# Performance work log

Measured on AMD Instinct MI355X. Metric: run time of the kernel, lower is better.

The kernel has to match this reference:

```python
import jax, jax.numpy as jnp
import numpy as np

X_DIM, H_DIM, Y_DIM, ROLLOUT = 256, 2048, 256, 4096


def setup_inputs() -> dict:
    key = jax.random.key(0)
    ks = jax.random.split(key, 6)
    inp = {
        "x": jax.random.normal(ks[0], (1, ROLLOUT, X_DIM), dtype=jnp.float32),
        "h": jnp.zeros((H_DIM,), dtype=jnp.float32),
        "Wc": jax.random.normal(ks[1], (X_DIM + H_DIM, H_DIM), dtype=jnp.float32) * 0.01,
        "Wu": jax.random.normal(ks[2], (X_DIM + H_DIM, H_DIM), dtype=jnp.float32) * 0.01,
        "Wr": jax.random.normal(ks[3], (X_DIM + H_DIM, H_DIM), dtype=jnp.float32) * 0.01,
        "bc": jnp.zeros((H_DIM,), dtype=jnp.float32),
        "bu": jnp.zeros((H_DIM,), dtype=jnp.float32),
        "br": jnp.zeros((H_DIM,), dtype=jnp.float32),
        "Wh_y": jax.random.normal(ks[4], (H_DIM, Y_DIM), dtype=jnp.float32) * 0.01,
        "by": jnp.zeros((Y_DIM,), dtype=jnp.float32),
    }
    return inp


def reference(x, h, Wc, Wu, Wr, bc, bu, br, Wh_y, by):
    xs = x[0]  # [T, x_dim]

    def step(hid, xt):
        xc = jnp.concatenate([xt, hid])                      # [x_dim + h_dim]
        Lu = jax.nn.sigmoid(xc @ Wu + bu)                    # update gate
        Lr = jax.nn.sigmoid(xc @ Wr + br)                    # reset gate
        xr = jnp.concatenate([xt, hid * Lr])
        c_tilda = jnp.tanh(xr @ Wc + bc)
        h_new = c_tilda * Lu + hid * (1.0 - Lu)
        y = h_new @ Wh_y + by
        return h_new, y

    h_fin, ys = jax.lax.scan(step, h, xs)  # ys: [T, y_dim]
    return ys, h_fin
```

## Files before the change

### kernel.cpp

```cpp
#include <hip/hip_runtime.h>
#include <hip/hip_bf16.h>

#define TSTEPS 4096
#define XD 256
#define HD 2048
#define YD 256
#define KD 2304
#define NWG 256
#define NT 512

#define WU_OFF 0
#define WR_OFF (8*KD*2)
#define WC_OFF (16*KD*2)
#define WY_OFF (24*KD*2)
#define V1_OFF (WY_OFF + HD*4)
#define V2_OFF (V1_OFF + KD*4)
#define RED_OFF (V2_OFF + KD*4)
#define LDS_BYTES (RED_OFF + 256)

#define HFLAGS_U32 0
#define RFLAGS_U32 8192
#define HGO_U32    16384
#define RGO_U32    16640
#define WS_ZERO_BYTES 67584
#define HB0_OFF 67584
#define HB1_OFF 75776
#define RB0_OFF 83968
#define RB1_OFF 92160

__device__ __forceinline__ float bflo(unsigned u){ return __uint_as_float(u << 16); }
__device__ __forceinline__ float bfhi(unsigned u){ return __uint_as_float(u & 0xffff0000u); }
__device__ __forceinline__ unsigned short f2bf(float f){
  unsigned b = __float_as_uint(f);
  b += 0x7fffu + ((b >> 16) & 1u);
  return (unsigned short)(b >> 16);
}
__device__ __forceinline__ float sigmoidf_(float x){ return 1.0f / (1.0f + __expf(-x)); }

__device__ __forceinline__ void gst32f(float* p, float v){
  __hip_atomic_store(p, v, __ATOMIC_RELAXED, __HIP_MEMORY_SCOPE_AGENT);
}
__device__ __forceinline__ void flagst(unsigned* p, unsigned v){
  __hip_atomic_store(p, v, __ATOMIC_RELAXED, __HIP_MEMORY_SCOPE_AGENT);
}
__device__ __forceinline__ void spinflag(const unsigned* p, unsigned epoch, long* budget){
  while (__hip_atomic_load(p, __ATOMIC_RELAXED, __HIP_MEMORY_SCOPE_AGENT) < epoch) {
    if (--(*budget) < 0) break;
    __builtin_amdgcn_s_sleep(1);
  }
}

__device__ __forceinline__ float4 cohload16(const float4* p){
  float4 r;
  asm volatile("global_load_dwordx4 %0, %1, off sc1\n\t"
               "s_waitcnt vmcnt(0)"
               : "=v"(r) : "v"(p) : "memory");
  return r;
}

__device__ __forceinline__ void relay_wait(unsigned* flags, unsigned* go,
                                           unsigned epoch, int wg, int tid, long* budget){
  if (wg == 0) {
    if (tid >= 1 && tid < NWG) spinflag(flags + tid*32, epoch, budget);
    __syncthreads();
    if (tid < 8) flagst(go + tid*32, epoch);
  } else {
    if (tid == 0) spinflag(go + (wg & 7)*32, epoch, budget);
    __syncthreads();
  }
}

template<int I0, int I1, int STRIDE>
__device__ __forceinline__ void dotacc(const float* v, const unsigned short* wcol,
                                       int lane, float4& acc){
  #pragma unroll
  for (int i = I0; i < I1; ++i) {
    int k = 4 * (lane + STRIDE * i);
    float4 vv = *(const float4*)(v + k);
    uint2  wq = *(const uint2*)(wcol + k);
    acc.x = fmaf(vv.x, bflo(wq.x), acc.x);
    acc.y = fmaf(vv.y, bfhi(wq.x), acc.y);
    acc.z = fmaf(vv.z, bflo(wq.y), acc.z);
    acc.w = fmaf(vv.w, bfhi(wq.y), acc.w);
  }
}

extern "C" __global__ void __launch_bounds__(NT)
gru_persistent(const float* __restrict__ x,  const float* __restrict__ h0,
               const float* __restrict__ Wc, const float* __restrict__ Wu,
               const float* __restrict__ Wr, const float* __restrict__ bc,
               const float* __restrict__ bu, const float* __restrict__ br,
               const float* __restrict__ Wy, const float* __restrict__ by,
               float* __restrict__ out, unsigned* wsu)
{
  extern __shared__ char smem[];
  unsigned short* wuS = (unsigned short*)(smem + WU_OFF);
  unsigned short* wrS = (unsigned short*)(smem + WR_OFF);
  unsigned short* wcS = (unsigned short*)(smem + WC_OFF);
  float* wyS = (float*)(smem + WY_OFF);
  float* v1  = (float*)(smem + V1_OFF);
  float* v2  = (float*)(smem + V2_OFF);
  float* red = (float*)(smem + RED_OFF);

  unsigned* hflags = wsu + HFLAGS_U32;
  unsigned* rflags = wsu + RFLAGS_U32;
  unsigned* hgo    = wsu + HGO_U32;
  unsigned* rgo    = wsu + RGO_U32;
  float* hb[2] = { (float*)((char*)wsu + HB0_OFF), (float*)((char*)wsu + HB1_OFF) };
  float* rb[2] = { (float*)((char*)wsu + RB0_OFF), (float*)((char*)wsu + RB1_OFF) };

  const int wg = blockIdx.x, tid = threadIdx.x;
  const int col0 = 8 * wg;

  for (int idx = tid; idx < 8*KD; idx += NT) {
    int c = idx & 7, k = idx >> 3;
    size_t g = (size_t)k * HD + col0 + c;
    wuS[c*KD + k] = f2bf(Wu[g]);
    wrS[c*KD + k] = f2bf(Wr[g]);
    wcS[c*KD + k] = f2bf(Wc[g]);
  }
  for (int k = tid; k < HD; k += NT) wyS[k] = Wy[(size_t)k * YD + wg];
  if (tid < 8) {
    red[16+tid] = bu[col0+tid];
    red[24+tid] = br[col0+tid];
    red[32+tid] = bc[col0+tid];
  }
  if (tid == 0) red[40] = by[wg];
  __syncthreads();

  long budget = 20000000;

  float4 xpref = make_float4(0.f, 0.f, 0.f, 0.f);
  if (tid < XD/4) xpref = ((const float4*)x)[tid];

  const int hw = tid >> 5, l = tid & 31, c = hw & 7;
  const int w  = tid >> 6, l6 = tid & 63;
  const unsigned short* wcol = ((hw < 8) ? wuS : wrS) + c * KD;
  const unsigned short* ccol = wcS + w * KD;

  for (int t = 0; t < TSTEPS; ++t) {
    if (tid < XD/4) {
      ((float4*)v1)[tid] = xpref;
      ((float4*)v2)[tid] = xpref;
    }
    __syncthreads();

    float4 a1 = make_float4(0.f, 0.f, 0.f, 0.f);
    dotacc<0, 2, 32>(v1, wcol, l, a1);

    if (t == 0) {
      ((float4*)(v1 + XD))[tid] = ((const float4*)h0)[tid];
      __syncthreads();
    } else {
      relay_wait(hflags, hgo, (unsigned)t, wg, tid, &budget);
      float4 hv = cohload16((const float4*)hb[(t+1)&1] + tid);
      ((float4*)(v1 + XD))[tid] = hv;
      __syncthreads();
    }

    dotacc<2, 18, 32>(v1, wcol, l, a1);
    {
      float s = (a1.x + a1.y) + (a1.z + a1.w);
      s += __shfl_xor(s, 16); s += __shfl_xor(s, 8); s += __shfl_xor(s, 4);
      s += __shfl_xor(s, 2);  s += __shfl_xor(s, 1);
      if (l == 0) {
        if (hw < 8) red[c] = sigmoidf_(s + red[16+c]);
        else gst32f(rb[t&1] + col0 + c, sigmoidf_(s + red[24+c]) * v1[XD+col0+c]);
      }
    }
    __syncthreads();
    if (tid == 0) flagst(rflags + wg*32, (unsigned)(t+1));

    {
      int k = 256 * w + 4 * l6;
      float4 hv  = *(const float4*)(v1 + XD + k);
      float4 wy4 = *(const float4*)(wyS + k);
      float ys = fmaf(hv.x, wy4.x, fmaf(hv.y, wy4.y, fmaf(hv.z, wy4.z, hv.w * wy4.w)));
      ys += __shfl_xor(ys, 32); ys += __shfl_xor(ys, 16); ys += __shfl_xor(ys, 8);
      ys += __shfl_xor(ys, 4);  ys += __shfl_xor(ys, 2);  ys += __shfl_xor(ys, 1);
      if (l6 == 0) red[8 + w] = ys;
    }
    if (tid < XD/4 && t + 1 < TSTEPS)
      xpref = ((const float4*)(x + (size_t)(t+1) * XD))[tid];

    relay_wait(rflags, rgo, (unsigned)(t+1), wg, tid, &budget);
    {
      float4 rv = cohload16((const float4*)rb[t&1] + tid);
      ((float4*)(v2 + XD))[tid] = rv;
    }
    __syncthreads();
    if (tid == 0 && t > 0) {
      float y = red[8]+red[9]+red[10]+red[11]+red[12]+red[13]+red[14]+red[15] + red[40];
      out[(size_t)(t-1) * YD + wg] = y;
    }

    {
      float4 a2 = make_float4(0.f, 0.f, 0.f, 0.f);
      dotacc<0, 9, 64>(v2, ccol, l6, a2);
      float s = (a2.x + a2.y) + (a2.z + a2.w);
      s += __shfl_xor(s, 32); s += __shfl_xor(s, 16); s += __shfl_xor(s, 8);
      s += __shfl_xor(s, 4);  s += __shfl_xor(s, 2);  s += __shfl_xor(s, 1);
      if (l6 == 0) {
        float cc = tanhf(s + red[32 + w]);
        float u  = red[w];
        float hp = v1[XD + col0 + w];
        gst32f(hb[t&1] + col0 + w, cc * u + hp * (1.0f - u));
      }
    }
    __syncthreads();
    if (tid == 0) flagst(hflags + wg*32, (unsigned)(t+1));
  }

  relay_wait(hflags, hgo, (unsigned)TSTEPS, wg, tid, &budget);
  {
    float4 hv = cohload16((const float4*)hb[(TSTEPS-1)&1] + tid);
    ((float4*)(v1 + XD))[tid] = hv;
  }
  __syncthreads();
  {
    int k = 256 * w + 4 * l6;
    float4 hv  = *(const float4*)(v1 + XD + k);
    float4 wy4 = *(const float4*)(wyS + k);
    float ys = fmaf(hv.x, wy4.x, fmaf(hv.y, wy4.y, fmaf(hv.z, wy4.z, hv.w * wy4.w)));
    ys += __shfl_xor(ys, 32); ys += __shfl_xor(ys, 16); ys += __shfl_xor(ys, 8);
    ys += __shfl_xor(ys, 4);  ys += __shfl_xor(ys, 2);  ys += __shfl_xor(ys, 1);
    if (l6 == 0) red[8 + w] = ys;
  }
  __syncthreads();
  if (tid == 0) {
    float y = red[8]+red[9]+red[10]+red[11]+red[12]+red[13]+red[14]+red[15] + red[40];
    out[(size_t)(TSTEPS-1) * YD + wg] = y;
  }
  if (tid < 8) out[(size_t)TSTEPS * YD + col0 + tid] = v1[XD + col0 + tid];
}

extern "C" void kernel_launch(void* const* d_in, const int* in_sizes, int n_in,
                              void* d_out, int out_size, void* d_ws, size_t ws_size,
                              hipStream_t stream) {
  const float* x  = (const float*)d_in[0];
  const float* h0 = (const float*)d_in[1];
  const float* Wc = (const float*)d_in[2];
  const float* Wu = (const float*)d_in[3];
  const float* Wr = (const float*)d_in[4];
  const float* bc = (const float*)d_in[5];
  const float* bu = (const float*)d_in[6];
  const float* br = (const float*)d_in[7];
  const float* Wy = (const float*)d_in[8];
  const float* by = (const float*)d_in[9];
  float* out = (float*)d_out;
  unsigned* wsu = (unsigned*)d_ws;

  hipFuncSetAttribute((const void*)gru_persistent,
                      hipFuncAttributeMaxDynamicSharedMemorySize, LDS_BYTES);
  hipMemsetAsync(d_ws, 0, WS_ZERO_BYTES, stream);
  gru_persistent<<<dim3(NWG), dim3(NT), LDS_BYTES, stream>>>(
      x, h0, Wc, Wu, Wr, bc, bu, br, Wy, by, out, wsu);
}
```

Baseline: 23.88 ms.

## Replace per-WG flag relay with sentinel-polled data buffers and a single-leader go broadcast

After: 25.07 ms. 5.0% more time.

```diff
diff --git a/kernel.cpp b/kernel.cpp
--- a/kernel.cpp
+++ b/kernel.cpp
@@ -18,15 +18,15 @@
 #define RED_OFF (V2_OFF + KD*4)
 #define LDS_BYTES (RED_OFF + 256)
 
-#define HFLAGS_U32 0
-#define RFLAGS_U32 8192
-#define HGO_U32    16384
-#define RGO_U32    16640
-#define WS_ZERO_BYTES 67584
-#define HB0_OFF 67584
-#define HB1_OFF 75776
-#define RB0_OFF 83968
-#define RB1_OFF 92160
+#define GOH_U32 0
+#define GOR_U32 256
+#define GO_BYTES 2048
+#define HB0_OFF 2048
+#define HB1_OFF 10240
+#define RB0_OFF 18432
+#define RB1_OFF 26624
+#define ARM_BYTES 32768
+#define SENT32 0x7F7F7F7Fu
 
 __device__ __forceinline__ float bflo(unsigned u){ return __uint_as_float(u << 16); }
 __device__ __forceinline__ float bfhi(unsigned u){ return __uint_as_float(u & 0xffff0000u); }
@@ -46,7 +46,6 @@
 __device__ __forceinline__ void spinflag(const unsigned* p, unsigned epoch, long* budget){
   while (__hip_atomic_load(p, __ATOMIC_RELAXED, __HIP_MEMORY_SCOPE_AGENT) < epoch) {
     if (--(*budget) < 0) break;
-    __builtin_amdgcn_s_sleep(1);
   }
 }
 
@@ -57,16 +56,24 @@
                : "=v"(r) : "v"(p) : "memory");
   return r;
 }
-
-__device__ __forceinline__ void relay_wait(unsigned* flags, unsigned* go,
-                                           unsigned epoch, int wg, int tid, long* budget){
-  if (wg == 0) {
-    if (tid >= 1 && tid < NWG) spinflag(flags + tid*32, epoch, budget);
-    __syncthreads();
-    if (tid < 8) flagst(go + tid*32, epoch);
-  } else {
-    if (tid == 0) spinflag(go + (wg & 7)*32, epoch, budget);
-    __syncthreads();
+__device__ __forceinline__ int has_sent(float4 v){
+  return (__float_as_uint(v.x) == SENT32) | (__float_as_uint(v.y) == SENT32) |
+         (__float_as_uint(v.z) == SENT32) | (__float_as_uint(v.w) == SENT32);
+}
+__device__ __forceinline__ float4 pollslice(const float4* p, long* budget){
+  float4 v = cohload16(p);
+  while (has_sent(v)) {
+    if (--(*budget) < 0) break;
+    v = cohload16(p);
+  }
+  return v;
+}
+__device__ __forceinline__ void reset_slice(float* gbuf, int col0, int tid){
+  if (tid < 2) {
+    unsigned long long s = 0x7F7F7F7F7F7F7F7FULL;
+    unsigned long long* p = (unsigned long long*)(gbuf + col0) + 2*tid;
+    __hip_atomic_store(p,     s, __ATOMIC_RELAXED, __HIP_MEMORY_SCOPE_AGENT);
+    __hip_atomic_store(p + 1, s, __ATOMIC_RELAXED, __HIP_MEMORY_SCOPE_AGENT);
   }
 }
 
@@ -102,10 +109,8 @@
   float* v2  = (float*)(smem + V2_OFF);
   float* red = (float*)(smem + RED_OFF);
 
-  unsigned* hflags = wsu + HFLAGS_U32;
-  unsigned* rflags = wsu + RFLAGS_U32;
-  unsigned* hgo    = wsu + HGO_U32;
-  unsigned* rgo    = wsu + RGO_U32;
+  unsigned* goh = wsu + GOH_U32;
+  unsigned* gor = wsu + GOR_U32;
   float* hb[2] = { (float*)((char*)wsu + HB0_OFF), (float*)((char*)wsu + HB1_OFF) };
   float* rb[2] = { (float*)((char*)wsu + RB0_OFF), (float*)((char*)wsu + RB1_OFF) };
 
@@ -139,23 +144,32 @@
   const unsigned short* ccol = wcS + w * KD;
 
   for (int t = 0; t < TSTEPS; ++t) {
-    if (tid < XD/4) {
-      ((float4*)v1)[tid] = xpref;
-      ((float4*)v2)[tid] = xpref;
-    }
-    __syncthreads();
-
     float4 a1 = make_float4(0.f, 0.f, 0.f, 0.f);
-    dotacc<0, 2, 32>(v1, wcol, l, a1);
 
     if (t == 0) {
+      if (tid < XD/4) { ((float4*)v1)[tid] = xpref; ((float4*)v2)[tid] = xpref; }
       ((float4*)(v1 + XD))[tid] = ((const float4*)h0)[tid];
       __syncthreads();
+      dotacc<0, 2, 32>(v1, wcol, l, a1);
+    } else if (wg == 0) {
+      float4 hv = pollslice((const float4*)hb[(t+1)&1] + tid, &budget);
+      ((float4*)(v1 + XD))[tid] = hv;
+      __syncthreads();
+      if (tid < 8) flagst(goh + tid*32, (unsigned)t);
+      if (tid < XD/4) { ((float4*)v1)[tid] = xpref; ((float4*)v2)[tid] = xpref; }
+      __syncthreads();
+      dotacc<0, 2, 32>(v1, wcol, l, a1);
+      if (t) reset_slice(rb[(t+1)&1], col0, tid);
     } else {
-      relay_wait(hflags, hgo, (unsigned)t, wg, tid, &budget);
+      if (tid < XD/4) { ((float4*)v1)[tid] = xpref; ((float4*)v2)[tid] = xpref; }
+      __syncthreads();
+      dotacc<0, 2, 32>(v1, wcol, l, a1);
+      if (tid == 0) spinflag(goh + (wg & 7)*32, (unsigned)t, &budget);
+      __syncthreads();
       float4 hv = cohload16((const float4*)hb[(t+1)&1] + tid);
       ((float4*)(v1 + XD))[tid] = hv;
       __syncthreads();
+      reset_slice(rb[(t+1)&1], col0, tid);
     }
 
     dotacc<2, 18, 32>(v1, wcol, l, a1);
@@ -168,35 +182,53 @@
         else gst32f(rb[t&1] + col0 + c, sigmoidf_(s + red[24+c]) * v1[XD+col0+c]);
       }
     }
-    __syncthreads();
-    if (tid == 0) flagst(rflags + wg*32, (unsigned)(t+1));
-
-    {
-      int k = 256 * w + 4 * l6;
-      float4 hv  = *(const float4*)(v1 + XD + k);
-      float4 wy4 = *(const float4*)(wyS + k);
-      float ys = fmaf(hv.x, wy4.x, fmaf(hv.y, wy4.y, fmaf(hv.z, wy4.z, hv.w * wy4.w)));
-      ys += __shfl_xor(ys, 32); ys += __shfl_xor(ys, 16); ys += __shfl_xor(ys, 8);
-      ys += __shfl_xor(ys, 4);  ys += __shfl_xor(ys, 2);  ys += __shfl_xor(ys, 1);
-      if (l6 == 0) red[8 + w] = ys;
-    }
-    if (tid < XD/4 && t + 1 < TSTEPS)
-      xpref = ((const float4*)(x + (size_t)(t+1) * XD))[tid];
-
-    relay_wait(rflags, rgo, (unsigned)(t+1), wg, tid, &budget);
-    {
+
+    float4 a2 = make_float4(0.f, 0.f, 0.f, 0.f);
+    if (wg == 0) {
+      float4 rv = pollslice((const float4*)rb[t&1] + tid, &budget);
+      ((float4*)(v2 + XD))[tid] = rv;
+      __syncthreads();
+      if (tid < 8) flagst(gor + tid*32, (unsigned)(t+1));
+      {
+        int k = 256 * w + 4 * l6;
+        float4 hv  = *(const float4*)(v1 + XD + k);
+        float4 wy4 = *(const float4*)(wyS + k);
+        float ys = fmaf(hv.x, wy4.x, fmaf(hv.y, wy4.y, fmaf(hv.z, wy4.z, hv.w * wy4.w)));
+        ys += __shfl_xor(ys, 32); ys += __shfl_xor(ys, 16); ys += __shfl_xor(ys, 8);
+        ys += __shfl_xor(ys, 4);  ys += __shfl_xor(ys, 2);  ys += __shfl_xor(ys, 1);
+        if (l6 == 0) red[8 + w] = ys;
+      }
+      dotacc<0, 1, 64>(v2, ccol, l6, a2);
+      if (tid < XD/4 && t + 1 < TSTEPS)
+        xpref = ((const float4*)(x + (size_t)(t+1) * XD))[tid];
+      __syncthreads();
+    } else {
+      {
+        int k = 256 * w + 4 * l6;
+        float4 hv  = *(const float4*)(v1 + XD + k);
+        float4 wy4 = *(const float4*)(wyS + k);
+        float ys = fmaf(hv.x, wy4.x, fmaf(hv.y, wy4.y, fmaf(hv.z, wy4.z, hv.w * wy4.w)));
+        ys += __shfl_xor(ys, 32); ys += __shfl_xor(ys, 16); ys += __shfl_xor(ys, 8);
+        ys += __shfl_xor(ys, 4);  ys += __shfl_xor(ys, 2);  ys += __shfl_xor(ys, 1);
+        if (l6 == 0) red[8 + w] = ys;
+      }
+      dotacc<0, 1, 64>(v2, ccol, l6, a2);
+      if (tid < XD/4 && t + 1 < TSTEPS)
+        xpref = ((const float4*)(x + (size_t)(t+1) * XD))[tid];
+      if (tid == 0) spinflag(gor + (wg & 7)*32, (unsigned)(t+1), &budget);
+      __syncthreads();
       float4 rv = cohload16((const float4*)rb[t&1] + tid);
       ((float4*)(v2 + XD))[tid] = rv;
-    }
-    __syncthreads();
+      __syncthreads();
+    }
+    if (t) reset_slice(hb[(t+1)&1], col0, tid);
     if (tid == 0 && t > 0) {
       float y = red[8]+red[9]+red[10]+red[11]+red[12]+red[13]+red[14]+red[15] + red[40];
       out[(size_t)(t-1) * YD + wg] = y;
     }
 
+    dotacc<1, 9, 64>(v2, ccol, l6, a2);
     {
-      float4 a2 = make_float4(0.f, 0.f, 0.f, 0.f);
-      dotacc<0, 9, 64>(v2, ccol, l6, a2);
       float s = (a2.x + a2.y) + (a2.z + a2.w);
       s += __shfl_xor(s, 32); s += __shfl_xor(s, 16); s += __shfl_xor(s, 8);
       s += __shfl_xor(s, 4);  s += __shfl_xor(s, 2);  s += __shfl_xor(s, 1);
@@ -208,11 +240,16 @@
       }
     }
     __syncthreads();
-    if (tid == 0) flagst(hflags + wg*32, (unsigned)(t+1));
-  }
-
-  relay_wait(hflags, hgo, (unsigned)TSTEPS, wg, tid, &budget);
-  {
+  }
+
+  if (wg == 0) {
+    float4 hv = pollslice((const float4*)hb[(TSTEPS-1)&1] + tid, &budget);
+    ((float4*)(v1 + XD))[tid] = hv;
+    __syncthreads();
+    if (tid < 8) flagst(goh + tid*32, (unsigned)TSTEPS);
+  } else {
+    if (tid == 0) spinflag(goh + (wg & 7)*32, (unsigned)TSTEPS, &budget);
+    __syncthreads();
     float4 hv = cohload16((const float4*)hb[(TSTEPS-1)&1] + tid);
     ((float4*)(v1 + XD))[tid] = hv;
   }
@@ -252,7 +289,8 @@
 
   hipFuncSetAttribute((const void*)gru_persistent,
                       hipFuncAttributeMaxDynamicSharedMemorySize, LDS_BYTES);
-  hipMemsetAsync(d_ws, 0, WS_ZERO_BYTES, stream);
+  hipMemsetAsync(d_ws, 0, GO_BYTES, stream);
+  hipMemsetAsync((char*)d_ws + GO_BYTES, 0x7F, ARM_BYTES, stream);
   gru_persistent<<<dim3(NWG), dim3(NT), LDS_BYTES, stream>>>(
       x, h0, Wc, Wu, Wr, bc, bu, br, Wy, by, out, wsu);
 }
```

## Replace relay-based grid barrier with atomic counter barrier and overlap x-part dot

Applied to the files above, without the earlier changes.

Result: slower. 40.14 ms (+68.1%).

```diff
diff --git a/kernel.cpp b/kernel.cpp
--- a/kernel.cpp
+++ b/kernel.cpp
@@ -18,15 +18,15 @@
 #define RED_OFF (V2_OFF + KD*4)
 #define LDS_BYTES (RED_OFF + 256)
 
-#define HFLAGS_U32 0
-#define RFLAGS_U32 8192
-#define HGO_U32    16384
-#define RGO_U32    16640
-#define WS_ZERO_BYTES 67584
-#define HB0_OFF 67584
-#define HB1_OFF 75776
-#define RB0_OFF 83968
-#define RB1_OFF 92160
+#define HCNT_OFF 0
+#define RCNT_OFF 128
+#define GOH_OFF  256
+#define GOR_OFF  1280
+#define WS_ZERO_BYTES 2304
+#define HB0_OFF 4096
+#define HB1_OFF 12288
+#define RB0_OFF 20480
+#define RB1_OFF 28672
 
 __device__ __forceinline__ float bflo(unsigned u){ return __uint_as_float(u << 16); }
 __device__ __forceinline__ float bfhi(unsigned u){ return __uint_as_float(u & 0xffff0000u); }
@@ -46,7 +46,13 @@
 __device__ __forceinline__ void spinflag(const unsigned* p, unsigned epoch, long* budget){
   while (__hip_atomic_load(p, __ATOMIC_RELAXED, __HIP_MEMORY_SCOPE_AGENT) < epoch) {
     if (--(*budget) < 0) break;
-    __builtin_amdgcn_s_sleep(1);
+  }
+}
+__device__ __forceinline__ void count_notify(unsigned* cnt, unsigned* go, unsigned epoch){
+  unsigned old = __hip_atomic_fetch_add(cnt, 1u, __ATOMIC_RELAXED, __HIP_MEMORY_SCOPE_AGENT);
+  if (old == epoch * NWG - 1u) {
+    #pragma unroll
+    for (int i = 0; i < 8; ++i) flagst(go + i*32, epoch);
   }
 }
 
@@ -56,18 +62,6 @@
                "s_waitcnt vmcnt(0)"
                : "=v"(r) : "v"(p) : "memory");
   return r;
-}
-
-__device__ __forceinline__ void relay_wait(unsigned* flags, unsigned* go,
-                                           unsigned epoch, int wg, int tid, long* budget){
-  if (wg == 0) {
-    if (tid >= 1 && tid < NWG) spinflag(flags + tid*32, epoch, budget);
-    __syncthreads();
-    if (tid < 8) flagst(go + tid*32, epoch);
-  } else {
-    if (tid == 0) spinflag(go + (wg & 7)*32, epoch, budget);
-    __syncthreads();
-  }
 }
 
 template<int I0, int I1, int STRIDE>
@@ -102,10 +96,10 @@
   float* v2  = (float*)(smem + V2_OFF);
   float* red = (float*)(smem + RED_OFF);
 
-  unsigned* hflags = wsu + HFLAGS_U32;
-  unsigned* rflags = wsu + RFLAGS_U32;
-  unsigned* hgo    = wsu + HGO_U32;
-  unsigned* rgo    = wsu + RGO_U32;
+  unsigned* hcnt = (unsigned*)((char*)wsu + HCNT_OFF);
+  unsigned* rcnt = (unsigned*)((char*)wsu + RCNT_OFF);
+  unsigned* goh  = (unsigned*)((char*)wsu + GOH_OFF);
+  unsigned* gor  = (unsigned*)((char*)wsu + GOR_OFF);
   float* hb[2] = { (float*)((char*)wsu + HB0_OFF), (float*)((char*)wsu + HB1_OFF) };
   float* rb[2] = { (float*)((char*)wsu + RB0_OFF), (float*)((char*)wsu + RB1_OFF) };
 
@@ -128,7 +122,7 @@
   if (tid == 0) red[40] = by[wg];
   __syncthreads();
 
-  long budget = 20000000;
+  long budget = 400000000;
 
   float4 xpref = make_float4(0.f, 0.f, 0.f, 0.f);
   if (tid < XD/4) xpref = ((const float4*)x)[tid];
@@ -152,7 +146,8 @@
       ((float4*)(v1 + XD))[tid] = ((const float4*)h0)[tid];
       __syncthreads();
     } else {
-      relay_wait(hflags, hgo, (unsigned)t, wg, tid, &budget);
+      if (tid == 0) spinflag(goh + (wg & 7)*32, (unsigned)t, &budget);
+      __syncthreads();
       float4 hv = cohload16((const float4*)hb[(t+1)&1] + tid);
       ((float4*)(v1 + XD))[tid] = hv;
       __syncthreads();
@@ -169,7 +164,7 @@
       }
     }
     __syncthreads();
-    if (tid == 0) flagst(rflags + wg*32, (unsigned)(t+1));
+    if (tid == 0) count_notify(rcnt, gor, (unsigned)(t+1));
 
     {
       int k = 256 * w + 4 * l6;
@@ -180,10 +175,13 @@
       ys += __shfl_xor(ys, 4);  ys += __shfl_xor(ys, 2);  ys += __shfl_xor(ys, 1);
       if (l6 == 0) red[8 + w] = ys;
     }
+    float4 a2 = make_float4(0.f, 0.f, 0.f, 0.f);
+    dotacc<0, 1, 64>(v2, ccol, l6, a2);
     if (tid < XD/4 && t + 1 < TSTEPS)
       xpref = ((const float4*)(x + (size_t)(t+1) * XD))[tid];
 
-    relay_wait(rflags, rgo, (unsigned)(t+1), wg, tid, &budget);
+    if (tid == 0) spinflag(gor + (wg & 7)*32, (unsigned)(t+1), &budget);
+    __syncthreads();
     {
       float4 rv = cohload16((const float4*)rb[t&1] + tid);
       ((float4*)(v2 + XD))[tid] = rv;
@@ -194,9 +192,8 @@
       out[(size_t)(t-1) * YD + wg] = y;
     }
 
-    {
-      float4 a2 = make_float4(0.f, 0.f, 0.f, 0.f);
-      dotacc<0, 9, 64>(v2, ccol, l6, a2);
+    dotacc<1, 9, 64>(v2, ccol, l6, a2);
+    {
       float s = (a2.x + a2.y) + (a2.z + a2.w);
       s += __shfl_xor(s, 32); s += __shfl_xor(s, 16); s += __shfl_xor(s, 8);
       s += __shfl_xor(s, 4);  s += __shfl_xor(s, 2);  s += __shfl_xor(s, 1);
@@ -208,12 +205,13 @@
       }
     }
     __syncthreads();
-    if (tid == 0) flagst(hflags + wg*32, (unsigned)(t+1));
-  }
-
-  relay_wait(hflags, hgo, (unsigned)TSTEPS, wg, tid, &budget);
+    if (tid == 0) count_notify(hcnt, goh, (unsigned)(t+1));
+  }
+
+  if (tid == 0) spinflag(goh + (wg & 7)*32, (unsigned)TSTEPS, &budget);
+  __syncthreads();
   {
-    float4 hv = cohload16((const float4*)hb[(TSTEPS-1)&1] + tid);
+    float4 hv = cohload16((const float4*)hb[(TSTEPS+1)&1] + tid);
     ((float4*)(v1 + XD))[tid] = hv;
   }
   __syncthreads();
```
